# Performance work log

Measured on AMD Instinct MI355X. Metric: run time of the kernel, lower is better.

The kernel has to match this reference:

```python
import jax, jax.numpy as jnp
import numpy as np

N_NODES = 100000
N_EDGES = 1600000
DIM = 128


def setup_inputs() -> dict:
    key = jax.random.key(0)
    ks = jax.random.split(key, 8)
    s = 1.0 / np.sqrt(DIM)
    return {
        "x": jax.random.normal(ks[0], (N_NODES, DIM), dtype=jnp.float32),
        "edge_index": jax.random.randint(ks[1], (2, N_EDGES), 0, N_NODES, dtype=jnp.int64),
        "W1_l": jax.random.normal(ks[2], (DIM, DIM), dtype=jnp.float32) * s,
        "b1": jnp.zeros((DIM,), dtype=jnp.float32),
        "W1_r": jax.random.normal(ks[3], (DIM, DIM), dtype=jnp.float32) * s,
        "W2_l": jax.random.normal(ks[4], (DIM, DIM), dtype=jnp.float32) * s,
        "b2": jnp.zeros((DIM,), dtype=jnp.float32),
        "W2_r": jax.random.normal(ks[5], (DIM, DIM), dtype=jnp.float32) * s,
    }


def _sage_conv(h, src, dst, n, W_l, b, W_r):
    # mean aggregation of source-node features onto target nodes
    agg = jax.ops.segment_sum(h[src], dst, num_segments=n)          # [N, D]
    deg = jax.ops.segment_sum(jnp.ones_like(src, dtype=h.dtype), dst, num_segments=n)
    agg = agg / jnp.maximum(deg, 1.0)[:, None]
    # PyG SAGEConv: lin_l(aggr) + bias + lin_r(x)  (root weight, no bias on lin_r)
    return agg @ W_l + b + h @ W_r


def reference(x, edge_index, W1_l, b1, W1_r, W2_l, b2, W2_r):
    src, dst = edge_index[0], edge_index[1]
    n = x.shape[0]
    h = jax.nn.relu(_sage_conv(x, src, dst, n, W1_l, b1, W1_r))
    return _sage_conv(h, src, dst, n, W2_l, b2, W2_r)
```

## Files before the change

### kernel.cpp

```cpp
#include <hip/hip_runtime.h>

typedef unsigned short ushort_t;
typedef unsigned int uint_t;

typedef short bf16x8 __attribute__((ext_vector_type(8)));
typedef float f32x4 __attribute__((ext_vector_type(4)));

#define DIM 128
#define BSHIFT 8
#define BNODES 256

__device__ __forceinline__ float bf2f(ushort_t u) {
    uint_t x = ((uint_t)u) << 16;
    float f;
    __builtin_memcpy(&f, &x, 4);
    return f;
}

__device__ __forceinline__ ushort_t f2bf(float f) {
    uint_t x;
    __builtin_memcpy(&x, &f, 4);
    uint_t r = (x + 0x7fffu + ((x >> 16) & 1u)) >> 16;
    return (ushort_t)r;
}


__global__ void k_cvt_f32_bf16(const float* __restrict__ in, ushort_t* __restrict__ out, int n4) {
    int i = blockIdx.x * blockDim.x + threadIdx.x;
    if (i < n4) {
        float4 f = ((const float4*)in)[i];
        ushort4 u;
        u.x = f2bf(f.x); u.y = f2bf(f.y); u.z = f2bf(f.z); u.w = f2bf(f.w);
        ((ushort4*)out)[i] = u;
    }
}

__global__ void k_wt4(const float* __restrict__ W0, const float* __restrict__ W1,
                      const float* __restrict__ W2, const float* __restrict__ W3,
                      ushort_t* __restrict__ T0, ushort_t* __restrict__ T1,
                      ushort_t* __restrict__ T2, ushort_t* __restrict__ T3) {
    int i = blockIdx.x * blockDim.x + threadIdx.x;
    int w = i >> 14, j = i & 16383;
    int n = j >> 7, k = j & 127;
    const float* W = (w == 0) ? W0 : (w == 1) ? W1 : (w == 2) ? W2 : W3;
    ushort_t* T = (w == 0) ? T0 : (w == 1) ? T1 : (w == 2) ? T2 : T3;
    T[j] = f2bf(W[k * DIM + n]);
}


__global__ __launch_bounds__(256) void k_bhist(const int* __restrict__ dst, int E, int NB,
                                               int* __restrict__ bucketCount) {
    __shared__ int hist[512];
    int t = threadIdx.x;
    for (int b = t; b < NB; b += 256) hist[b] = 0;
    __syncthreads();
    int per = (E + gridDim.x - 1) / gridDim.x;
    int beg = blockIdx.x * per, end = min(beg + per, E);
    for (int i = beg + t; i < end; i += 256)
        atomicAdd(&hist[dst[i] >> BSHIFT], 1);
    __syncthreads();
    for (int b = t; b < NB; b += 256) {
        int v = hist[b];
        if (v) atomicAdd(&bucketCount[b], v);
    }
}

__global__ __launch_bounds__(512) void k_bscan(const int* __restrict__ bucketCount, int NB, int E,
                                               int* __restrict__ bucketBase,
                                               int* __restrict__ bucketCursor,
                                               int* __restrict__ row_ptr, int N) {
    __shared__ int lds[512];
    int t = threadIdx.x;
    int v = (t < NB) ? bucketCount[t] : 0;
    lds[t] = v;
    __syncthreads();
    for (int off = 1; off < 512; off <<= 1) {
        int u = (t >= off) ? lds[t - off] : 0;
        __syncthreads();
        lds[t] += u;
        __syncthreads();
    }
    if (t < NB) {
        int b = lds[t] - v;
        bucketBase[t] = b;
        bucketCursor[t] = b;
    }
    if (t == 0) row_ptr[N] = E;
}

__global__ __launch_bounds__(256) void k_bucketize(const int* __restrict__ src,
                                                   const int* __restrict__ dst, int E, int NB,
                                                   int* __restrict__ bucketCursor,
                                                   uint_t* __restrict__ bebuf) {
    __shared__ int hist[512];
    __shared__ int base[512];
    int t = threadIdx.x;
    for (int b = t; b < NB; b += 256) hist[b] = 0;
    __syncthreads();
    int per = (E + gridDim.x - 1) / gridDim.x;
    int beg = blockIdx.x * per, end = min(beg + per, E);
    for (int i = beg + t; i < end; i += 256)
        atomicAdd(&hist[dst[i] >> BSHIFT], 1);
    __syncthreads();
    for (int b = t; b < NB; b += 256) {
        int v = hist[b];
        base[b] = v ? atomicAdd(&bucketCursor[b], v) : 0;
        hist[b] = 0;
    }
    __syncthreads();
    for (int i = beg + t; i < end; i += 256) {
        int d = dst[i], s = src[i];
        int b = d >> BSHIFT;
        int off = atomicAdd(&hist[b], 1);
        bebuf[base[b] + off] = ((uint_t)(d & (BNODES - 1)) << 24) | (uint_t)s;
    }
}

__global__ __launch_bounds__(256) void k_bcsr(const uint_t* __restrict__ bebuf,
                                              const int* __restrict__ bucketBase,
                                              const int* __restrict__ bucketCount, int N,
                                              int* __restrict__ row_ptr, int* __restrict__ csr) {
    __shared__ int hist[BNODES];
    __shared__ int cur[BNODES];
    int t = threadIdx.x;
    int b = blockIdx.x;
    int ebase = bucketBase[b], cnt = bucketCount[b];
    int nodeBase = b << BSHIFT;
    hist[t] = 0;
    __syncthreads();
    for (int i = t; i < cnt; i += 256)
        atomicAdd(&hist[bebuf[ebase + i] >> 24], 1);
    __syncthreads();
    int v = hist[t];
    for (int off = 1; off < 256; off <<= 1) {
        int u = (t >= off) ? hist[t - off] : 0;
        __syncthreads();
        hist[t] += u;
        __syncthreads();
    }
    int excl = hist[t] - v;
    int node = nodeBase + t;
    if (node < N) row_ptr[node] = ebase + excl;
    cur[t] = excl;
    __syncthreads();
    for (int i = t; i < cnt; i += 256) {
        uint_t e = bebuf[ebase + i];
        int dl = (int)(e >> 24);
        int pos = atomicAdd(&cur[dl], 1);
        csr[ebase + pos] = (int)(e & 0xFFFFFFu);
    }
}


__device__ __forceinline__ void acc8(float* a, uint4 p) {
    a[0] += bf2f((ushort_t)(p.x & 0xffffu));
    a[1] += bf2f((ushort_t)(p.x >> 16));
    a[2] += bf2f((ushort_t)(p.y & 0xffffu));
    a[3] += bf2f((ushort_t)(p.y >> 16));
    a[4] += bf2f((ushort_t)(p.z & 0xffffu));
    a[5] += bf2f((ushort_t)(p.z >> 16));
    a[6] += bf2f((ushort_t)(p.w & 0xffffu));
    a[7] += bf2f((ushort_t)(p.w >> 16));
}

__global__ __launch_bounds__(256) void k_agg(const ushort_t* __restrict__ X,
                                             const int* __restrict__ row_ptr,
                                             const int* __restrict__ csr,
                                             ushort_t* __restrict__ out, int n) {
    int node = (int)((blockIdx.x * (unsigned)blockDim.x + threadIdx.x) >> 4);
    if (node >= n) return;
    int sl = threadIdx.x & 15;
    int beg = row_ptr[node], end = row_ptr[node + 1];
    float a[8] = {0.f, 0.f, 0.f, 0.f, 0.f, 0.f, 0.f, 0.f};

    int e = beg;
    for (; e + 4 <= end; e += 4) {
        int s0 = csr[e + 0], s1 = csr[e + 1], s2 = csr[e + 2], s3 = csr[e + 3];
        uint4 p0 = *(const uint4*)(X + (size_t)s0 * DIM + sl * 8);
        uint4 p1 = *(const uint4*)(X + (size_t)s1 * DIM + sl * 8);
        uint4 p2 = *(const uint4*)(X + (size_t)s2 * DIM + sl * 8);
        uint4 p3 = *(const uint4*)(X + (size_t)s3 * DIM + sl * 8);
        acc8(a, p0); acc8(a, p1); acc8(a, p2); acc8(a, p3);
    }
    for (; e < end; e++) {
        int s = csr[e];
        uint4 p = *(const uint4*)(X + (size_t)s * DIM + sl * 8);
        acc8(a, p);
    }

    int cnt = end - beg;
    float sc = (cnt > 0) ? 1.f / (float)cnt : 0.f;
    uint4 o;
    o.x = (uint_t)f2bf(a[0] * sc) | ((uint_t)f2bf(a[1] * sc) << 16);
    o.y = (uint_t)f2bf(a[2] * sc) | ((uint_t)f2bf(a[3] * sc) << 16);
    o.z = (uint_t)f2bf(a[4] * sc) | ((uint_t)f2bf(a[5] * sc) << 16);
    o.w = (uint_t)f2bf(a[6] * sc) | ((uint_t)f2bf(a[7] * sc) << 16);
    *(uint4*)(out + (size_t)node * DIM + sl * 8) = o;
}


template <bool RELU, bool OUT_BF16>
__global__ __launch_bounds__(256) void k_gemm(const ushort_t* __restrict__ A1,
                                              const ushort_t* __restrict__ A2,
                                              const ushort_t* __restrict__ WTl,
                                              const ushort_t* __restrict__ WTr,
                                              const float* __restrict__ bias,
                                              void* __restrict__ Out, int n_waves, int M) {
    __shared__ ushort_t sW[2 * 128 * 128];
    int t = threadIdx.x;
    int wave = (int)((blockIdx.x * 256u + t) >> 6);
    int lane = t & 63;
    int col = lane & 15;
    int quad = lane >> 4;
    bool active = (wave < n_waves);

    bf16x8 a[2][8];
    if (active) {
#pragma unroll
        for (int tt = 0; tt < 2; tt++) {
            int arow = wave * 32 + tt * 16 + col;
            const ushort_t* a1p = A1 + (size_t)arow * DIM + quad * 8;
            const ushort_t* a2p = A2 + (size_t)arow * DIM + quad * 8;
#pragma unroll
            for (int ks = 0; ks < 4; ks++) a[tt][ks] = *(const bf16x8*)(a1p + ks * 32);
#pragma unroll
            for (int ks = 0; ks < 4; ks++) a[tt][4 + ks] = *(const bf16x8*)(a2p + ks * 32);
        }
    }

    {
        int tab = t >> 7, row = t & 127;
        const ushort_t* g = (tab ? WTr : WTl) + (size_t)row * 128;
        ushort_t* d = sW + (size_t)t * 128;
        int sw = row & 15;
#pragma unroll
        for (int c = 0; c < 16; c++) {
            uint4 v = *(const uint4*)(g + c * 8);
            *(uint4*)(d + ((c ^ sw) * 8)) = v;
        }
    }
    __syncthreads();
    if (!active) return;

    f32x4 acc[2][8];
#pragma unroll
    for (int tt = 0; tt < 2; tt++)
#pragma unroll
        for (int nt = 0; nt < 8; nt++) acc[tt][nt] = (f32x4){0.f, 0.f, 0.f, 0.f};

    const ushort_t* sWl = sW;
    const ushort_t* sWr = sW + 128 * 128;
#pragma unroll
    for (int nt = 0; nt < 8; nt++) {
        int row = nt * 16 + col;
        const ushort_t* bl = sWl + (size_t)row * 128;
        const ushort_t* br = sWr + (size_t)row * 128;
#pragma unroll
        for (int ks = 0; ks < 4; ks++) {
            bf16x8 b = *(const bf16x8*)(bl + (((ks * 4 + quad) ^ col) * 8));
            acc[0][nt] = __builtin_amdgcn_mfma_f32_16x16x32_bf16(a[0][ks], b, acc[0][nt], 0, 0, 0);
            acc[1][nt] = __builtin_amdgcn_mfma_f32_16x16x32_bf16(a[1][ks], b, acc[1][nt], 0, 0, 0);
        }
#pragma unroll
        for (int ks = 0; ks < 4; ks++) {
            bf16x8 b = *(const bf16x8*)(br + (((ks * 4 + quad) ^ col) * 8));
            acc[0][nt] = __builtin_amdgcn_mfma_f32_16x16x32_bf16(a[0][4 + ks], b, acc[0][nt], 0, 0, 0);
            acc[1][nt] = __builtin_amdgcn_mfma_f32_16x16x32_bf16(a[1][4 + ks], b, acc[1][nt], 0, 0, 0);
        }
    }

#pragma unroll
    for (int tt = 0; tt < 2; tt++)
#pragma unroll
        for (int nt = 0; nt < 8; nt++) {
            int c = nt * 16 + col;
            float bv = bias[c];
#pragma unroll
            for (int r = 0; r < 4; r++) {
                int m = wave * 32 + tt * 16 + quad * 4 + r;
                if (m < M) {
                    float v = acc[tt][nt][r] + bv;
                    if (RELU) v = v > 0.f ? v : 0.f;
                    if (OUT_BF16)
                        ((ushort_t*)Out)[(size_t)m * DIM + c] = f2bf(v);
                    else
                        ((float*)Out)[(size_t)m * DIM + c] = v;
                }
            }
        }
}


extern "C" void kernel_launch(void* const* d_in, const int* in_sizes, int n_in,
                              void* d_out, int out_size, void* d_ws, size_t ws_size,
                              hipStream_t stream) {
    const int N = in_sizes[0] / DIM;
    const int E = in_sizes[1] / 2;
    const int NB = (N + BNODES - 1) >> BSHIFT;

    const float* x   = (const float*)d_in[0];
    const int*   ei  = (const int*)d_in[1];
    const int*   src = ei;
    const int*   dst = ei + E;
    const float* W1l = (const float*)d_in[2];
    const float* b1  = (const float*)d_in[3];
    const float* W1r = (const float*)d_in[4];
    const float* W2l = (const float*)d_in[5];
    const float* b2  = (const float*)d_in[6];
    const float* W2r = (const float*)d_in[7];
    float* out = (float*)d_out;

    char* ws = (char*)d_ws;
    size_t off = 0;
    auto alloc = [&](size_t bytes) -> char* {
        char* p = ws + off;
        off = (off + bytes + 255) & ~(size_t)255;
        return p;
    };

    int*      bucketCount  = (int*)alloc((size_t)NB * 4);
    int*      bucketBase   = (int*)alloc((size_t)NB * 4);
    int*      bucketCursor = (int*)alloc((size_t)NB * 4);
    int*      row_ptr      = (int*)alloc((size_t)(N + 1) * 4);
    int*      csr          = (int*)alloc((size_t)E * 4);
    uint_t*   bebuf        = (uint_t*)alloc((size_t)E * 4);
    size_t    fpad         = (size_t)32 * DIM * 2;
    ushort_t* xb           = (ushort_t*)alloc((size_t)N * DIM * 2 + fpad);
    ushort_t* hb           = (ushort_t*)alloc((size_t)N * DIM * 2 + fpad);
    ushort_t* aggb         = (ushort_t*)alloc((size_t)N * DIM * 2 + fpad);
    ushort_t* wt1l         = (ushort_t*)alloc((size_t)DIM * DIM * 2);
    ushort_t* wt1r         = (ushort_t*)alloc((size_t)DIM * DIM * 2);
    ushort_t* wt2l         = (ushort_t*)alloc((size_t)DIM * DIM * 2);
    ushort_t* wt2r         = (ushort_t*)alloc((size_t)DIM * DIM * 2);

    hipMemsetAsync(bucketCount, 0, (size_t)NB * 4, stream);

    {
        int n4 = N * DIM / 4;
        k_cvt_f32_bf16<<<dim3((n4 + 255) / 256), dim3(256), 0, stream>>>(x, xb, n4);
    }
    k_wt4<<<dim3(4 * DIM * DIM / 256), dim3(256), 0, stream>>>(W1l, W1r, W2l, W2r,
                                                               wt1l, wt1r, wt2l, wt2r);
    k_bhist<<<dim3(256), dim3(256), 0, stream>>>(dst, E, NB, bucketCount);
    k_bscan<<<dim3(1), dim3(512), 0, stream>>>(bucketCount, NB, E, bucketBase, bucketCursor, row_ptr, N);
    k_bucketize<<<dim3(256), dim3(256), 0, stream>>>(src, dst, E, NB, bucketCursor, bebuf);
    k_bcsr<<<dim3(NB), dim3(256), 0, stream>>>(bebuf, bucketBase, bucketCount, N, row_ptr, csr);

    const int n_waves = (N + 31) / 32;
    dim3 gemm_grid((n_waves + 3) / 4), gemm_blk(256);
    dim3 agg_grid((N + 15) / 16), agg_blk(256);

    k_agg<<<agg_grid, agg_blk, 0, stream>>>(xb, row_ptr, csr, aggb, N);
    k_gemm<true, true><<<gemm_grid, gemm_blk, 0, stream>>>(aggb, xb, wt1l, wt1r, b1, hb, n_waves, N);
    k_agg<<<agg_grid, agg_blk, 0, stream>>>(hb, row_ptr, csr, aggb, N);
    k_gemm<false, false><<<gemm_grid, gemm_blk, 0, stream>>>(aggb, hb, wt2l, wt2r, b2, out, n_waves, N);

    (void)n_in; (void)out_size; (void)ws_size;
}
```

Baseline: 357.8 us.

## Store features in column-chunked layout and sort nodes by degree for aggregation

Bf16 feature matrices are stored as 8 column chunks of 16 features each, and the aggregation grid is split per chunk. Each chunk's gather then touches a 3.2 MB slice that may stay resident in cache, rather than scattered 256-byte rows across the whole matrix. Nodes are also bucketed by degree via a histogram, scan and scatter permutation, so threads in a block do similar amounts of work. The GEMM loads and bf16 stores are rewritten for the chunked layout. The cost is three extra preprocessing kernels, 32-byte gathers with more index reloads per chunk (each csr entry is now read 8 times), and the removal of row-padding slack.

Result: slower. 584.2 us (+63.3%).

```diff
diff --git a/kernel.cpp b/kernel.cpp
--- a/kernel.cpp
+++ b/kernel.cpp
@@ -5,10 +5,12 @@
 
 typedef short bf16x8 __attribute__((ext_vector_type(8)));
 typedef float f32x4 __attribute__((ext_vector_type(4)));
+typedef uint_t uint4v __attribute__((ext_vector_type(4)));
 
 #define DIM 128
 #define BSHIFT 8
 #define BNODES 256
+#define NCHUNK 8
 
 __device__ __forceinline__ float bf2f(ushort_t u) {
     uint_t x = ((uint_t)u) << 16;
@@ -25,14 +27,20 @@
 }
 
 
-__global__ void k_cvt_f32_bf16(const float* __restrict__ in, ushort_t* __restrict__ out, int n4) {
+__global__ __launch_bounds__(256) void k_cvt_chunk(const float* __restrict__ in,
+                                                   ushort_t* __restrict__ out, int N) {
     int i = blockIdx.x * blockDim.x + threadIdx.x;
-    if (i < n4) {
-        float4 f = ((const float4*)in)[i];
-        ushort4 u;
-        u.x = f2bf(f.x); u.y = f2bf(f.y); u.z = f2bf(f.z); u.w = f2bf(f.w);
-        ((ushort4*)out)[i] = u;
-    }
+    if (i >= N * 16) return;
+    int node = i >> 4, q = i & 15;
+    const float4* p = (const float4*)(in + (size_t)node * DIM + q * 8);
+    float4 f0 = p[0], f1 = p[1];
+    uint4v o;
+    o.x = (uint_t)f2bf(f0.x) | ((uint_t)f2bf(f0.y) << 16);
+    o.y = (uint_t)f2bf(f0.z) | ((uint_t)f2bf(f0.w) << 16);
+    o.z = (uint_t)f2bf(f1.x) | ((uint_t)f2bf(f1.y) << 16);
+    o.w = (uint_t)f2bf(f1.z) | ((uint_t)f2bf(f1.w) << 16);
+    size_t CS = (size_t)N * 16;
+    *(uint4v*)(out + (size_t)(q >> 1) * CS + (size_t)node * 16 + (q & 1) * 8) = o;
 }
 
 __global__ void k_wt4(const float* __restrict__ W0, const float* __restrict__ W1,
@@ -152,7 +160,69 @@
 }
 
 
-__device__ __forceinline__ void acc8(float* a, uint4 p) {
+__global__ __launch_bounds__(256) void k_dhist(const int* __restrict__ rp, int N,
+                                               int* __restrict__ degCount) {
+    __shared__ int h[256];
+    int t = threadIdx.x;
+    h[t] = 0;
+    __syncthreads();
+    int i = blockIdx.x * 256 + t;
+    if (i < N) {
+        int d = rp[i + 1] - rp[i];
+        atomicAdd(&h[d > 255 ? 255 : d], 1);
+    }
+    __syncthreads();
+    int v = h[t];
+    if (v) atomicAdd(&degCount[t], v);
+}
+
+__global__ __launch_bounds__(256) void k_dscan(const int* __restrict__ degCount,
+                                               int* __restrict__ classBase,
+                                               int* __restrict__ classCursor) {
+    __shared__ int lds[256];
+    int t = threadIdx.x;
+    int v = degCount[t];
+    lds[t] = v;
+    __syncthreads();
+    for (int off = 1; off < 256; off <<= 1) {
+        int u = (t >= off) ? lds[t - off] : 0;
+        __syncthreads();
+        lds[t] += u;
+        __syncthreads();
+    }
+    int b = lds[t] - v;
+    classBase[t] = b;
+    classCursor[t] = b;
+}
+
+__global__ __launch_bounds__(256) void k_dscatter(const int* __restrict__ rp, int N,
+                                                  int* __restrict__ classCursor,
+                                                  int* __restrict__ perm) {
+    __shared__ int h[256];
+    __shared__ int base[256];
+    int t = threadIdx.x;
+    h[t] = 0;
+    __syncthreads();
+    int i = blockIdx.x * 256 + t;
+    int cls = 0;
+    if (i < N) {
+        int d = rp[i + 1] - rp[i];
+        cls = d > 255 ? 255 : d;
+        atomicAdd(&h[cls], 1);
+    }
+    __syncthreads();
+    int v = h[t];
+    base[t] = v ? atomicAdd(&classCursor[t], v) : 0;
+    h[t] = 0;
+    __syncthreads();
+    if (i < N) {
+        int r = atomicAdd(&h[cls], 1);
+        perm[base[cls] + r] = i;
+    }
+}
+
+
+__device__ __forceinline__ void acc8v(float* a, uint4v p) {
     a[0] += bf2f((ushort_t)(p.x & 0xffffu));
     a[1] += bf2f((ushort_t)(p.x >> 16));
     a[2] += bf2f((ushort_t)(p.y & 0xffffu));
@@ -163,39 +233,51 @@
     a[7] += bf2f((ushort_t)(p.w >> 16));
 }
 
-__global__ __launch_bounds__(256) void k_agg(const ushort_t* __restrict__ X,
-                                             const int* __restrict__ row_ptr,
-                                             const int* __restrict__ csr,
-                                             ushort_t* __restrict__ out, int n) {
-    int node = (int)((blockIdx.x * (unsigned)blockDim.x + threadIdx.x) >> 4);
-    if (node >= n) return;
-    int sl = threadIdx.x & 15;
-    int beg = row_ptr[node], end = row_ptr[node + 1];
+__global__ __launch_bounds__(256) void k_agg_c(const ushort_t* __restrict__ X,
+                                               const int* __restrict__ rp,
+                                               const int* __restrict__ csr,
+                                               const int* __restrict__ perm,
+                                               ushort_t* __restrict__ out, int N) {
+    int chunk = blockIdx.x & 7;
+    int g = blockIdx.x >> 3;
+    int t = threadIdx.x;
+    int idx = g * 128 + (t >> 1);
+    if (idx >= N) return;
+    int node = perm[idx];
+    int half = t & 1;
+    size_t CS = (size_t)N * 16;
+    const ushort_t* Xc = X + (size_t)chunk * CS;
+
+    int beg = __builtin_nontemporal_load(rp + node);
+    int end = __builtin_nontemporal_load(rp + node + 1);
     float a[8] = {0.f, 0.f, 0.f, 0.f, 0.f, 0.f, 0.f, 0.f};
 
     int e = beg;
     for (; e + 4 <= end; e += 4) {
-        int s0 = csr[e + 0], s1 = csr[e + 1], s2 = csr[e + 2], s3 = csr[e + 3];
-        uint4 p0 = *(const uint4*)(X + (size_t)s0 * DIM + sl * 8);
-        uint4 p1 = *(const uint4*)(X + (size_t)s1 * DIM + sl * 8);
-        uint4 p2 = *(const uint4*)(X + (size_t)s2 * DIM + sl * 8);
-        uint4 p3 = *(const uint4*)(X + (size_t)s3 * DIM + sl * 8);
-        acc8(a, p0); acc8(a, p1); acc8(a, p2); acc8(a, p3);
+        int s0 = __builtin_nontemporal_load(csr + e + 0);
+        int s1 = __builtin_nontemporal_load(csr + e + 1);
+        int s2 = __builtin_nontemporal_load(csr + e + 2);
+        int s3 = __builtin_nontemporal_load(csr + e + 3);
+        uint4v p0 = *(const uint4v*)(Xc + (size_t)s0 * 16 + half * 8);
+        uint4v p1 = *(const uint4v*)(Xc + (size_t)s1 * 16 + half * 8);
+        uint4v p2 = *(const uint4v*)(Xc + (size_t)s2 * 16 + half * 8);
+        uint4v p3 = *(const uint4v*)(Xc + (size_t)s3 * 16 + half * 8);
+        acc8v(a, p0); acc8v(a, p1); acc8v(a, p2); acc8v(a, p3);
     }
     for (; e < end; e++) {
-        int s = csr[e];
-        uint4 p = *(const uint4*)(X + (size_t)s * DIM + sl * 8);
-        acc8(a, p);
+        int s = __builtin_nontemporal_load(csr + e);
+        uint4v p = *(const uint4v*)(Xc + (size_t)s * 16 + half * 8);
+        acc8v(a, p);
     }
 
     int cnt = end - beg;
     float sc = (cnt > 0) ? 1.f / (float)cnt : 0.f;
-    uint4 o;
+    uint4v o;
     o.x = (uint_t)f2bf(a[0] * sc) | ((uint_t)f2bf(a[1] * sc) << 16);
     o.y = (uint_t)f2bf(a[2] * sc) | ((uint_t)f2bf(a[3] * sc) << 16);
     o.z = (uint_t)f2bf(a[4] * sc) | ((uint_t)f2bf(a[5] * sc) << 16);
     o.w = (uint_t)f2bf(a[6] * sc) | ((uint_t)f2bf(a[7] * sc) << 16);
-    *(uint4*)(out + (size_t)node * DIM + sl * 8) = o;
+    __builtin_nontemporal_store(o, (uint4v*)(out + (size_t)chunk * CS + (size_t)node * 16 + half * 8));
 }
 
 
@@ -213,18 +295,21 @@
     int col = lane & 15;
     int quad = lane >> 4;
     bool active = (wave < n_waves);
+    size_t CS = (size_t)M * 16;
 
     bf16x8 a[2][8];
     if (active) {
 #pragma unroll
         for (int tt = 0; tt < 2; tt++) {
             int arow = wave * 32 + tt * 16 + col;
-            const ushort_t* a1p = A1 + (size_t)arow * DIM + quad * 8;
-            const ushort_t* a2p = A2 + (size_t)arow * DIM + quad * 8;
-#pragma unroll
-            for (int ks = 0; ks < 4; ks++) a[tt][ks] = *(const bf16x8*)(a1p + ks * 32);
-#pragma unroll
-            for (int ks = 0; ks < 4; ks++) a[tt][4 + ks] = *(const bf16x8*)(a2p + ks * 32);
+            size_t rbase = (size_t)arow * 16 + (quad & 1) * 8;
+            size_t cbase = (size_t)(quad >> 1) * CS;
+#pragma unroll
+            for (int ks = 0; ks < 4; ks++)
+                a[tt][ks] = *(const bf16x8*)(A1 + cbase + (size_t)(ks * 2) * CS + rbase);
+#pragma unroll
+            for (int ks = 0; ks < 4; ks++)
+                a[tt][4 + ks] = *(const bf16x8*)(A2 + cbase + (size_t)(ks * 2) * CS + rbase);
         }
     }
 
@@ -282,7 +367,7 @@
                     float v = acc[tt][nt][r] + bv;
                     if (RELU) v = v > 0.f ? v : 0.f;
                     if (OUT_BF16)
-                        ((ushort_t*)Out)[(size_t)m * DIM + c] = f2bf(v);
+                        ((ushort_t*)Out)[(size_t)nt * CS + (size_t)m * 16 + col] = f2bf(v);
                     else
                         ((float*)Out)[(size_t)m * DIM + c] = v;
                 }
@@ -321,38 +406,46 @@
     int*      bucketCount  = (int*)alloc((size_t)NB * 4);
     int*      bucketBase   = (int*)alloc((size_t)NB * 4);
     int*      bucketCursor = (int*)alloc((size_t)NB * 4);
+    int*      degCount     = (int*)alloc(256 * 4);
+    int*      classBase    = (int*)alloc(256 * 4);
+    int*      classCursor  = (int*)alloc(256 * 4);
+    int*      perm         = (int*)alloc((size_t)N * 4);
     int*      row_ptr      = (int*)alloc((size_t)(N + 1) * 4);
     int*      csr          = (int*)alloc((size_t)E * 4);
     uint_t*   bebuf        = (uint_t*)alloc((size_t)E * 4);
-    size_t    fpad         = (size_t)32 * DIM * 2;
-    ushort_t* xb           = (ushort_t*)alloc((size_t)N * DIM * 2 + fpad);
-    ushort_t* hb           = (ushort_t*)alloc((size_t)N * DIM * 2 + fpad);
-    ushort_t* aggb         = (ushort_t*)alloc((size_t)N * DIM * 2 + fpad);
+    ushort_t* xb           = (ushort_t*)alloc((size_t)N * DIM * 2);
+    ushort_t* hb           = (ushort_t*)alloc((size_t)N * DIM * 2);
+    ushort_t* aggb         = (ushort_t*)alloc((size_t)N * DIM * 2);
     ushort_t* wt1l         = (ushort_t*)alloc((size_t)DIM * DIM * 2);
     ushort_t* wt1r         = (ushort_t*)alloc((size_t)DIM * DIM * 2);
     ushort_t* wt2l         = (ushort_t*)alloc((size_t)DIM * DIM * 2);
     ushort_t* wt2r         = (ushort_t*)alloc((size_t)DIM * DIM * 2);
 
     hipMemsetAsync(bucketCount, 0, (size_t)NB * 4, stream);
-
-    {
-        int n4 = N * DIM / 4;
-        k_cvt_f32_bf16<<<dim3((n4 + 255) / 256), dim3(256), 0, stream>>>(x, xb, n4);
-    }
+    hipMemsetAsync(degCount, 0, 256 * 4, stream);
+
+    k_cvt_chunk<<<dim3((N * 16 + 255) / 256), dim3(256), 0, stream>>>(x, xb, N);
     k_wt4<<<dim3(4 * DIM * DIM / 256), dim3(256), 0, stream>>>(W1l, W1r, W2l, W2r,
                                                                wt1l, wt1r, wt2l, wt2r);
     k_bhist<<<dim3(256), dim3(256), 0, stream>>>(dst, E, NB, bucketCount);
     k_bscan<<<dim3(1), dim3(512), 0, stream>>>(bucketCount, NB, E, bucketBase, bucketCursor, row_ptr, N);
     k_bucketize<<<dim3(256), dim3(256), 0, stream>>>(src, dst, E, NB, bucketCursor, bebuf);
     k_bcsr<<<dim3(NB), dim3(256), 0, stream>>>(bebuf, bucketBase, bucketCount, N, row_ptr, csr);
+    {
+        int nblk = (N + 255) / 256;
+        k_dhist<<<dim3(nblk), dim3(256), 0, stream>>>(row_ptr, N, degCount);
+        k_dscan<<<dim3(1), dim3(256), 0, stream>>>(degCount, classBase, classCursor);
+        k_dscatter<<<dim3(nblk), dim3(256), 0, stream>>>(row_ptr, N, classCursor, perm);
+    }
 
     const int n_waves = (N + 31) / 32;
     dim3 gemm_grid((n_waves + 3) / 4), gemm_blk(256);
-    dim3 agg_grid((N + 15) / 16), agg_blk(256);
-
-    k_agg<<<agg_grid, agg_blk, 0, stream>>>(xb, row_ptr, csr, aggb, N);
+    const int ngrp = (N + 127) / 128;
+    dim3 agg_grid(ngrp * NCHUNK), agg_blk(256);
+
+    k_agg_c<<<agg_grid, agg_blk, 0, stream>>>(xb, row_ptr, csr, perm, aggb, N);
     k_gemm<true, true><<<gemm_grid, gemm_blk, 0, stream>>>(aggb, xb, wt1l, wt1r, b1, hb, n_waves, N);
-    k_agg<<<agg_grid, agg_blk, 0, stream>>>(hb, row_ptr, csr, aggb, N);
+    k_agg_c<<<agg_grid, agg_blk, 0, stream>>>(hb, row_ptr, csr, perm, aggb, N);
     k_gemm<false, false><<<gemm_grid, gemm_blk, 0, stream>>>(aggb, hb, wt2l, wt2r, b2, out, n_waves, N);
 
     (void)n_in; (void)out_size; (void)ws_size;
```

## Sort nodes by degree for load-balanced aggregation and unroll gather by 8

Applied to the files above, without the earlier changes.

Adds a degree histogram, scan and scatter pass that builds a permutation of nodes grouped by in-degree. The aggregation kernels then process nodes in that order so each wave's 16-lane groups have similar edge counts, reducing divergence and tail imbalance. The gather loop also gets an 8-wide unrolled stage to keep more loads in flight. The cost is three extra small kernels, an indirect perm lookup, and output writes scattered in node order, which lose some locality.

Result: slower. 376.0 us (+5.1%).

```diff
diff --git a/kernel.cpp b/kernel.cpp
--- a/kernel.cpp
+++ b/kernel.cpp
@@ -152,6 +152,68 @@
 }
 
 
+__global__ __launch_bounds__(256) void k_dhist(const int* __restrict__ rp, int N,
+                                               int* __restrict__ degCount) {
+    __shared__ int h[256];
+    int t = threadIdx.x;
+    h[t] = 0;
+    __syncthreads();
+    int i = blockIdx.x * 256 + t;
+    if (i < N) {
+        int d = rp[i + 1] - rp[i];
+        atomicAdd(&h[d > 255 ? 255 : d], 1);
+    }
+    __syncthreads();
+    int v = h[t];
+    if (v) atomicAdd(&degCount[t], v);
+}
+
+__global__ __launch_bounds__(256) void k_dscan(const int* __restrict__ degCount,
+                                               int* __restrict__ classBase,
+                                               int* __restrict__ classCursor) {
+    __shared__ int lds[256];
+    int t = threadIdx.x;
+    int v = degCount[t];
+    lds[t] = v;
+    __syncthreads();
+    for (int off = 1; off < 256; off <<= 1) {
+        int u = (t >= off) ? lds[t - off] : 0;
+        __syncthreads();
+        lds[t] += u;
+        __syncthreads();
+    }
+    int b = lds[t] - v;
+    classBase[t] = b;
+    classCursor[t] = b;
+}
+
+__global__ __launch_bounds__(256) void k_dscatter(const int* __restrict__ rp, int N,
+                                                  int* __restrict__ classCursor,
+                                                  int* __restrict__ perm) {
+    __shared__ int h[256];
+    __shared__ int base[256];
+    int t = threadIdx.x;
+    h[t] = 0;
+    __syncthreads();
+    int i = blockIdx.x * 256 + t;
+    int cls = 0;
+    if (i < N) {
+        int d = rp[i + 1] - rp[i];
+        cls = d > 255 ? 255 : d;
+        atomicAdd(&h[cls], 1);
+    }
+    __syncthreads();
+    int v = h[t];
+    base[t] = v ? atomicAdd(&classCursor[t], v) : 0;
+    h[t] = 0;
+    __syncthreads();
+    if (i < N) {
+        int r = atomicAdd(&h[cls], 1);
+        perm[base[cls] + r] = i;
+    }
+}
+
+
 __device__ __forceinline__ void acc8(float* a, uint4 p) {
     a[0] += bf2f((ushort_t)(p.x & 0xffffu));
     a[1] += bf2f((ushort_t)(p.x >> 16));
@@ -166,14 +228,30 @@
 __global__ __launch_bounds__(256) void k_agg(const ushort_t* __restrict__ X,
                                              const int* __restrict__ row_ptr,
                                              const int* __restrict__ csr,
+                                             const int* __restrict__ perm,
                                              ushort_t* __restrict__ out, int n) {
-    int node = (int)((blockIdx.x * (unsigned)blockDim.x + threadIdx.x) >> 4);
-    if (node >= n) return;
+    int idx = (int)((blockIdx.x * (unsigned)blockDim.x + threadIdx.x) >> 4);
+    if (idx >= n) return;
+    int node = perm[idx];
     int sl = threadIdx.x & 15;
     int beg = row_ptr[node], end = row_ptr[node + 1];
     float a[8] = {0.f, 0.f, 0.f, 0.f, 0.f, 0.f, 0.f, 0.f};
 
     int e = beg;
+    for (; e + 8 <= end; e += 8) {
+        int s0 = csr[e + 0], s1 = csr[e + 1], s2 = csr[e + 2], s3 = csr[e + 3];
+        int s4 = csr[e + 4], s5 = csr[e + 5], s6 = csr[e + 6], s7 = csr[e + 7];
+        uint4 p0 = *(const uint4*)(X + (size_t)s0 * DIM + sl * 8);
+        uint4 p1 = *(const uint4*)(X + (size_t)s1 * DIM + sl * 8);
+        uint4 p2 = *(const uint4*)(X + (size_t)s2 * DIM + sl * 8);
+        uint4 p3 = *(const uint4*)(X + (size_t)s3 * DIM + sl * 8);
+        uint4 p4 = *(const uint4*)(X + (size_t)s4 * DIM + sl * 8);
+        uint4 p5 = *(const uint4*)(X + (size_t)s5 * DIM + sl * 8);
+        uint4 p6 = *(const uint4*)(X + (size_t)s6 * DIM + sl * 8);
+        uint4 p7 = *(const uint4*)(X + (size_t)s7 * DIM + sl * 8);
+        acc8(a, p0); acc8(a, p1); acc8(a, p2); acc8(a, p3);
+        acc8(a, p4); acc8(a, p5); acc8(a, p6); acc8(a, p7);
+    }
     for (; e + 4 <= end; e += 4) {
         int s0 = csr[e + 0], s1 = csr[e + 1], s2 = csr[e + 2], s3 = csr[e + 3];
         uint4 p0 = *(const uint4*)(X + (size_t)s0 * DIM + sl * 8);
@@ -321,6 +399,10 @@
     int*      bucketCount  = (int*)alloc((size_t)NB * 4);
     int*      bucketBase   = (int*)alloc((size_t)NB * 4);
     int*      bucketCursor = (int*)alloc((size_t)NB * 4);
+    int*      degCount     = (int*)alloc(256 * 4);
+    int*      classBase    = (int*)alloc(256 * 4);
+    int*      classCursor  = (int*)alloc(256 * 4);
+    int*      perm         = (int*)alloc((size_t)N * 4);
     int*      row_ptr      = (int*)alloc((size_t)(N + 1) * 4);
     int*      csr          = (int*)alloc((size_t)E * 4);
     uint_t*   bebuf        = (uint_t*)alloc((size_t)E * 4);
@@ -334,6 +416,7 @@
     ushort_t* wt2r         = (ushort_t*)alloc((size_t)DIM * DIM * 2);
 
     hipMemsetAsync(bucketCount, 0, (size_t)NB * 4, stream);
+    hipMemsetAsync(degCount, 0, 256 * 4, stream);
 
     {
         int n4 = N * DIM / 4;
@@ -345,14 +428,20 @@
     k_bscan<<<dim3(1), dim3(512), 0, stream>>>(bucketCount, NB, E, bucketBase, bucketCursor, row_ptr, N);
     k_bucketize<<<dim3(256), dim3(256), 0, stream>>>(src, dst, E, NB, bucketCursor, bebuf);
     k_bcsr<<<dim3(NB), dim3(256), 0, stream>>>(bebuf, bucketBase, bucketCount, N, row_ptr, csr);
+    {
+        int nblk = (N + 255) / 256;
+        k_dhist<<<dim3(nblk), dim3(256), 0, stream>>>(row_ptr, N, degCount);
+        k_dscan<<<dim3(1), dim3(256), 0, stream>>>(degCount, classBase, classCursor);
+        k_dscatter<<<dim3(nblk), dim3(256), 0, stream>>>(row_ptr, N, classCursor, perm);
+    }
 
     const int n_waves = (N + 31) / 32;
     dim3 gemm_grid((n_waves + 3) / 4), gemm_blk(256);
     dim3 agg_grid((N + 15) / 16), agg_blk(256);
 
-    k_agg<<<agg_grid, agg_blk, 0, stream>>>(xb, row_ptr, csr, aggb, N);
+    k_agg<<<agg_grid, agg_blk, 0, stream>>>(xb, row_ptr, csr, perm, aggb, N);
     k_gemm<true, true><<<gemm_grid, gemm_blk, 0, stream>>>(aggb, xb, wt1l, wt1r, b1, hb, n_waves, N);
-    k_agg<<<agg_grid, agg_blk, 0, stream>>>(hb, row_ptr, csr, aggb, N);
+    k_agg<<<agg_grid, agg_blk, 0, stream>>>(hb, row_ptr, csr, perm, aggb, N);
     k_gemm<false, false><<<gemm_grid, gemm_blk, 0, stream>>>(aggb, hb, wt2l, wt2r, b2, out, n_waves, N);
 
     (void)n_in; (void)out_size; (void)ws_size;
```
